# Performance work log

Hardware: AMD Instinct MI355X
Metric: run time of the kernel (lower is better)

## Reference

```python
import jax, jax.numpy as jnp
import numpy as np
from jax import lax

B, T, F_IN, H = 256, 800, 3, 200  # batch, time_steps, n_features, n_hidden=time_steps//4


def hard_sigmoid(z):
    return jnp.clip(0.2 * z + 0.5, 0.0, 1.0)


def lstm_hardsigmoid(x_btf, Wih, Whh, bih, bhh):
    """Unidirectional single-layer LSTM, hard-sigmoid gates, zero init state.
    x_btf: (B, T, F); Wih: (4H, F); Whh: (4H, H); biases: (4H,). Returns (B, T, H)."""
    Hh = Whh.shape[1]
    # input contribution for all timesteps at once: (B, T, 4H)
    pre = jnp.einsum('btf,gf->btg', x_btf, Wih) + bih + bhh
    pre_tb = jnp.swapaxes(pre, 0, 1)  # (T, B, 4H)
    b = x_btf.shape[0]
    init = (jnp.zeros((b, Hh), x_btf.dtype), jnp.zeros((b, Hh), x_btf.dtype))

    def step(carry, pre_t):
        h, c = carry
        gates = pre_t + h @ Whh.T  # (B, 4H)
        i, f, g, o = jnp.split(gates, 4, axis=-1)  # torch gate order i,f,g,o
        i = hard_sigmoid(i)
        f = hard_sigmoid(f)
        g = jnp.tanh(g)
        o = hard_sigmoid(o)
        c_new = f * c + i * g
        h_new = o * jnp.tanh(c_new)
        return (h_new, c_new), h_new

    _, hs = lax.scan(step, init, pre_tb)  # hs: (T, B, H)
    return jnp.swapaxes(hs, 0, 1)


def setup_inputs() -> dict:
    key = jax.random.key(0)
    ks = jax.random.split(key, 4)
    return {
        'x': jax.random.normal(ks[0], (B, F_IN, T), jnp.float32),
        'enc_Wih': jax.random.normal(ks[1], (4 * H, F_IN), jnp.float32) * 0.1,
        'enc_Whh': jax.random.normal(ks[2], (4 * H, H), jnp.float32) * 0.05,
        'enc_bih': jnp.zeros((4 * H,), jnp.float32),
        'enc_bhh': jnp.zeros((4 * H,), jnp.float32),
        'dec_Wih': jax.random.normal(ks[3], (4 * F_IN, H), jnp.float32) * 0.05,
        'dec_Whh': jax.random.normal(jax.random.fold_in(key, 7), (4 * F_IN, F_IN), jnp.float32) * 0.1,
        'dec_bih': jnp.zeros((4 * F_IN,), jnp.float32),
        'dec_bhh': jnp.zeros((4 * F_IN,), jnp.float32),
    }


def reference(x, enc_Wih, enc_Whh, enc_bih, enc_bhh, dec_Wih, dec_Whh, dec_bih, dec_bhh):
    # x: (B, n_features, T) -> permute -> (B, T, n_features)
    xi = jnp.transpose(x, (0, 2, 1))
    enc_out = lstm_hardsigmoid(xi, enc_Wih, enc_Whh, enc_bih, enc_bhh)  # (B, T, H)
    # max_pool1d over time (kernel = full length) == max over T
    pooled = jnp.max(enc_out, axis=1)  # (B, H)
    # repeat pooled vector for every timestep
    dec_in = jnp.broadcast_to(pooled[:, None, :], (pooled.shape[0], T, H))
    dec_out = lstm_hardsigmoid(dec_in, dec_Wih, dec_Whh, dec_bih, dec_bhh)  # (B, T, F)
    return jnp.transpose(dec_out, (0, 2, 1))  # (B, n_features, T)
```

## Files before the change

### kernel.cpp

```cpp
#include <hip/hip_runtime.h>
#include <hip/hip_fp16.h>
#include <stdint.h>


typedef _Float16 half2_t __attribute__((ext_vector_type(2)));

__device__ __forceinline__ float fdot2f(uint32_t hp, uint32_t wp, float acc) {
#if __has_builtin(__builtin_amdgcn_fdot2)
  return __builtin_amdgcn_fdot2(__builtin_bit_cast(half2_t, hp),
                                __builtin_bit_cast(half2_t, wp), acc, false);
#else
  half2_t a = __builtin_bit_cast(half2_t, hp);
  half2_t b = __builtin_bit_cast(half2_t, wp);
  return acc + (float)a[0] * (float)b[0] + (float)a[1] * (float)b[1];
#endif
}

__device__ __forceinline__ float hsig(float z) {
  return fminf(fmaxf(__builtin_fmaf(0.2f, z, 0.5f), 0.f), 1.f);
}

__device__ __forceinline__ float tanh_fast(float v) {
  float e = __builtin_amdgcn_exp2f(v * 2.885390081777927f);
  return 1.f - 2.f * __builtin_amdgcn_rcpf(e + 1.f);
}

__global__ void prep_kernel(const float* __restrict__ whh,
                            uint32_t* __restrict__ wpk) {
  int idx = blockIdx.x * 256 + threadIdx.x;
  if (idx >= 80000) return;
  int p = idx / 800;
  int j = idx - p * 800;
  float a = whh[j * 200 + 2 * p];
  float b = whh[j * 200 + 2 * p + 1];
  __half2 v = __floats2half2_rn(a, b);
  wpk[idx] = __builtin_bit_cast(uint32_t, v);
}

__global__ __launch_bounds__(832, 1)
void enc_kernel(const float* __restrict__ x,
                const float* __restrict__ wih,
                const float* __restrict__ bih,
                const float* __restrict__ bhh,
                const uint32_t* __restrict__ wpk,
                const float* __restrict__ dwih,
                const float* __restrict__ dbih,
                const float* __restrict__ dbhh,
                const float* __restrict__ dwhh,
                float* __restrict__ out)
{
  const int b = blockIdx.x;
  const int t = threadIdx.x;

  __shared__ float xs[2400];
  __shared__ alignas(16) __half hh[200];
  __shared__ float gates[800];
  __shared__ float pooled[200];
  __shared__ float pre12s[12];
  __shared__ int s_tc;

  for (int i = t; i < 2400; i += 832) xs[i] = x[(size_t)b * 2400 + i];
  if (t < 200) hh[t] = __float2half(0.f);

  const bool worker = t < 800;
  const int gtype = t / 200;
  uint32_t w[100];
  float bias = 0.f, wi0 = 0.f, wi1 = 0.f, wi2 = 0.f;
  if (worker) {
#pragma unroll
    for (int p = 0; p < 100; ++p) w[p] = wpk[p * 800 + t];
    bias = bih[t] + bhh[t];
    wi0 = wih[t * 3 + 0]; wi1 = wih[t * 3 + 1]; wi2 = wih[t * 3 + 2];
  }
  float c_state = 0.f;
  float maxh = -INFINITY;
  __syncthreads();

  for (int step = 0; step < 800; ++step) {
    if (worker) {
      float a0 = 0.f, a1 = 0.f;
      const uint4* H4 = (const uint4*)hh;
#pragma unroll
      for (int q = 0; q < 25; ++q) {
        uint4 Hv = H4[q];
        a0 = fdot2f(Hv.x, w[4 * q + 0], a0);
        a1 = fdot2f(Hv.y, w[4 * q + 1], a1);
        a0 = fdot2f(Hv.z, w[4 * q + 2], a0);
        a1 = fdot2f(Hv.w, w[4 * q + 3], a1);
      }
      float g = a0 + a1 + bias;
      g = __builtin_fmaf(wi0, xs[step], g);
      g = __builtin_fmaf(wi1, xs[800 + step], g);
      g = __builtin_fmaf(wi2, xs[1600 + step], g);
      float act;
      if (gtype == 2) act = tanh_fast(g); else act = hsig(g);
      gates[t] = act;
    }
    __syncthreads();
    if (t < 200) {
      float ai = gates[t], af = gates[t + 200];
      float ag = gates[t + 400], ao = gates[t + 600];
      c_state = __builtin_fmaf(af, c_state, ai * ag);
      float h_ = ao * tanh_fast(c_state);
      maxh = fmaxf(maxh, h_);
      hh[t] = __float2half(h_);
    }
    __syncthreads();
  }

  if (t < 200) pooled[t] = maxh;
  __syncthreads();
  if (t < 12) {
    float s = dbih[t] + dbhh[t];
    const float* wr = dwih + t * 200;
#pragma unroll 8
    for (int u = 0; u < 200; ++u) s = __builtin_fmaf(pooled[u], wr[u], s);
    pre12s[t] = s;
  }
  __syncthreads();

  if (t < 3) {
    float pre[12];
#pragma unroll
    for (int j = 0; j < 12; ++j) pre[j] = pre12s[j];
    float W[36];
#pragma unroll
    for (int j = 0; j < 36; ++j) W[j] = dwhh[j];

    float h0 = 0, h1 = 0, h2 = 0, c0 = 0, c1 = 0, c2 = 0;
    int tc = 800;
    float* hist = xs + t * 800;
    for (int step = 0; step < 800; ++step) {
      float g[12];
#pragma unroll
      for (int j = 0; j < 12; ++j) {
        float v = pre[j];
        v = __builtin_fmaf(W[j * 3 + 0], h0, v);
        v = __builtin_fmaf(W[j * 3 + 1], h1, v);
        v = __builtin_fmaf(W[j * 3 + 2], h2, v);
        g[j] = v;
      }
      float nc0 = hsig(g[3]) * c0 + hsig(g[0]) * tanh_fast(g[6]);
      float nc1 = hsig(g[4]) * c1 + hsig(g[1]) * tanh_fast(g[7]);
      float nc2 = hsig(g[5]) * c2 + hsig(g[2]) * tanh_fast(g[8]);
      float nh0 = hsig(g[9])  * tanh_fast(nc0);
      float nh1 = hsig(g[10]) * tanh_fast(nc1);
      float nh2 = hsig(g[11]) * tanh_fast(nc2);
      bool same = (nh0 == h0) && (nh1 == h1) && (nh2 == h2) &&
                  (nc0 == c0) && (nc1 == c1) && (nc2 == c2);
      float mine = (t == 0) ? nh0 : ((t == 1) ? nh1 : nh2);
      hist[step] = mine;
      h0 = nh0; h1 = nh1; h2 = nh2; c0 = nc0; c1 = nc1; c2 = nc2;
      if (same) { tc = step + 1; break; }
    }
    if (t == 0) s_tc = tc;
  }
  __syncthreads();

  {
    const int tc1 = s_tc - 1;
    float* ob = out + (size_t)b * 2400;
    if (t < 800) {
      int idx = (t < s_tc) ? t : tc1;
      ob[t]        = xs[idx];
      ob[800 + t]  = xs[800 + idx];
      ob[1600 + t] = xs[1600 + idx];
    }
  }
}

extern "C" void kernel_launch(void* const* d_in, const int* in_sizes, int n_in,
                              void* d_out, int out_size, void* d_ws, size_t ws_size,
                              hipStream_t stream)
{
  const float* x    = (const float*)d_in[0];
  const float* wih  = (const float*)d_in[1];
  const float* whh  = (const float*)d_in[2];
  const float* bih  = (const float*)d_in[3];
  const float* bhh  = (const float*)d_in[4];
  const float* dwih = (const float*)d_in[5];
  const float* dwhh = (const float*)d_in[6];
  const float* dbih = (const float*)d_in[7];
  const float* dbhh = (const float*)d_in[8];
  float* out = (float*)d_out;

  uint32_t* wpk = (uint32_t*)d_ws;

  hipLaunchKernelGGL(prep_kernel, dim3(313), dim3(256), 0, stream, whh, wpk);
  hipLaunchKernelGGL(enc_kernel, dim3(256), dim3(832), 0, stream,
                     x, wih, bih, bhh, wpk, dwih, dbih, dbhh, dwhh, out);
}
```

Before: 1.205 ms.

## Compute all four gates per hidden unit in one thread with double-buffered h

The encoder now uses 200 worker threads instead of 800. Each thread holds the weights of all four gates for one hidden unit in registers, about 400 words, and computes the cell update itself. This removes the shared gates array and the second barrier each step, and the h vector is double-buffered so one barrier per step is enough. The inputs are packed as float4 per timestep. The risks are heavy register pressure and possible spills, plus only one wave per SIMD left to hide latency.

```diff
diff --git a/kernel.cpp b/kernel.cpp
--- a/kernel.cpp
+++ b/kernel.cpp
@@ -37,7 +37,7 @@
   wpk[idx] = __builtin_bit_cast(uint32_t, v);
 }
 
-__global__ __launch_bounds__(832, 1)
+__global__ __launch_bounds__(256, 1)
 void enc_kernel(const float* __restrict__ x,
                 const float* __restrict__ wih,
                 const float* __restrict__ bih,
@@ -52,63 +52,91 @@
   const int b = blockIdx.x;
   const int t = threadIdx.x;
 
-  __shared__ float xs[2400];
-  __shared__ alignas(16) __half hh[200];
-  __shared__ float gates[800];
+  __shared__ alignas(16) float xs[3200];
+  __shared__ alignas(16) __half hh[2][208];
   __shared__ float pooled[200];
   __shared__ float pre12s[12];
   __shared__ int s_tc;
 
-  for (int i = t; i < 2400; i += 832) xs[i] = x[(size_t)b * 2400 + i];
-  if (t < 200) hh[t] = __float2half(0.f);
-
-  const bool worker = t < 800;
-  const int gtype = t / 200;
-  uint32_t w[100];
-  float bias = 0.f, wi0 = 0.f, wi1 = 0.f, wi2 = 0.f;
+  {
+    const float* xb = x + (size_t)b * 2400;
+    float4* X4 = (float4*)xs;
+    for (int tt = t; tt < 800; tt += 256) {
+      float4 v;
+      v.x = xb[tt];
+      v.y = xb[800 + tt];
+      v.z = xb[1600 + tt];
+      v.w = 0.f;
+      X4[tt] = v;
+    }
+  }
+  if (t < 208) { hh[0][t] = __float2half(0.f); }
+
+  const bool worker = t < 200;
+  uint32_t w[400];
+  float bias[4] = {0, 0, 0, 0};
+  float wi[12];
+#pragma unroll
+  for (int j = 0; j < 12; ++j) wi[j] = 0.f;
   if (worker) {
 #pragma unroll
-    for (int p = 0; p < 100; ++p) w[p] = wpk[p * 800 + t];
-    bias = bih[t] + bhh[t];
-    wi0 = wih[t * 3 + 0]; wi1 = wih[t * 3 + 1]; wi2 = wih[t * 3 + 2];
+    for (int g = 0; g < 4; ++g) {
+      const int row = t + 200 * g;
+#pragma unroll
+      for (int p = 0; p < 100; ++p) w[g * 100 + p] = wpk[p * 800 + row];
+      bias[g] = bih[row] + bhh[row];
+      wi[g * 3 + 0] = wih[row * 3 + 0];
+      wi[g * 3 + 1] = wih[row * 3 + 1];
+      wi[g * 3 + 2] = wih[row * 3 + 2];
+    }
   }
   float c_state = 0.f;
   float maxh = -INFINITY;
   __syncthreads();
 
+  int cur = 0;
   for (int step = 0; step < 800; ++step) {
     if (worker) {
-      float a0 = 0.f, a1 = 0.f;
-      const uint4* H4 = (const uint4*)hh;
+      float acc[8];
+#pragma unroll
+      for (int j = 0; j < 8; ++j) acc[j] = 0.f;
+      const uint4* H4 = (const uint4*)hh[cur];
 #pragma unroll
       for (int q = 0; q < 25; ++q) {
         uint4 Hv = H4[q];
-        a0 = fdot2f(Hv.x, w[4 * q + 0], a0);
-        a1 = fdot2f(Hv.y, w[4 * q + 1], a1);
-        a0 = fdot2f(Hv.z, w[4 * q + 2], a0);
-        a1 = fdot2f(Hv.w, w[4 * q + 3], a1);
+        const int d = q & 1;
+#pragma unroll
+        for (int g = 0; g < 4; ++g) {
+          float a = acc[2 * g + d];
+          a = fdot2f(Hv.x, w[g * 100 + 4 * q + 0], a);
+          a = fdot2f(Hv.y, w[g * 100 + 4 * q + 1], a);
+          a = fdot2f(Hv.z, w[g * 100 + 4 * q + 2], a);
+          a = fdot2f(Hv.w, w[g * 100 + 4 * q + 3], a);
+          acc[2 * g + d] = a;
+        }
       }
-      float g = a0 + a1 + bias;
-      g = __builtin_fmaf(wi0, xs[step], g);
-      g = __builtin_fmaf(wi1, xs[800 + step], g);
-      g = __builtin_fmaf(wi2, xs[1600 + step], g);
-      float act;
-      if (gtype == 2) act = tanh_fast(g); else act = hsig(g);
-      gates[t] = act;
+      float4 xv = ((const float4*)xs)[step];
+      float gte[4];
+#pragma unroll
+      for (int g = 0; g < 4; ++g) {
+        float v = acc[2 * g] + acc[2 * g + 1] + bias[g];
+        v = __builtin_fmaf(wi[g * 3 + 0], xv.x, v);
+        v = __builtin_fmaf(wi[g * 3 + 1], xv.y, v);
+        v = __builtin_fmaf(wi[g * 3 + 2], xv.z, v);
+        gte[g] = v;
+      }
+      float i_ = hsig(gte[0]), f_ = hsig(gte[1]), o_ = hsig(gte[3]);
+      float g_ = tanh_fast(gte[2]);
+      c_state = __builtin_fmaf(f_, c_state, i_ * g_);
+      float h_ = o_ * tanh_fast(c_state);
+      maxh = fmaxf(maxh, h_);
+      hh[cur ^ 1][t] = __float2half(h_);
     }
     __syncthreads();
-    if (t < 200) {
-      float ai = gates[t], af = gates[t + 200];
-      float ag = gates[t + 400], ao = gates[t + 600];
-      c_state = __builtin_fmaf(af, c_state, ai * ag);
-      float h_ = ao * tanh_fast(c_state);
-      maxh = fmaxf(maxh, h_);
-      hh[t] = __float2half(h_);
-    }
-    __syncthreads();
-  }
-
-  if (t < 200) pooled[t] = maxh;
+    cur ^= 1;
+  }
+
+  if (worker) pooled[t] = maxh;
   __syncthreads();
   if (t < 12) {
     float s = dbih[t] + dbhh[t];
@@ -129,7 +157,6 @@
 
     float h0 = 0, h1 = 0, h2 = 0, c0 = 0, c1 = 0, c2 = 0;
     int tc = 800;
-    float* hist = xs + t * 800;
     for (int step = 0; step < 800; ++step) {
       float g[12];
 #pragma unroll
@@ -149,7 +176,7 @@
       bool same = (nh0 == h0) && (nh1 == h1) && (nh2 == h2) &&
                   (nc0 == c0) && (nc1 == c1) && (nc2 == c2);
       float mine = (t == 0) ? nh0 : ((t == 1) ? nh1 : nh2);
-      hist[step] = mine;
+      xs[step * 4 + t] = mine;
       h0 = nh0; h1 = nh1; h2 = nh2; c0 = nc0; c1 = nc1; c2 = nc2;
       if (same) { tc = step + 1; break; }
     }
@@ -158,13 +185,13 @@
   __syncthreads();
 
   {
-    const int tc1 = s_tc - 1;
+    const int tcv = s_tc, tc1 = tcv - 1;
     float* ob = out + (size_t)b * 2400;
-    if (t < 800) {
-      int idx = (t < s_tc) ? t : tc1;
-      ob[t]        = xs[idx];
-      ob[800 + t]  = xs[800 + idx];
-      ob[1600 + t] = xs[1600 + idx];
+    for (int tt = t; tt < 800; tt += 256) {
+      int idx = (tt < tcv) ? tt : tc1;
+      ob[tt]        = xs[idx * 4 + 0];
+      ob[800 + tt]  = xs[idx * 4 + 1];
+      ob[1600 + tt] = xs[idx * 4 + 2];
     }
   }
 }
@@ -187,6 +214,6 @@
   uint32_t* wpk = (uint32_t*)d_ws;
 
   hipLaunchKernelGGL(prep_kernel, dim3(313), dim3(256), 0, stream, whh, wpk);
-  hipLaunchKernelGGL(enc_kernel, dim3(256), dim3(832), 0, stream,
+  hipLaunchKernelGGL(enc_kernel, dim3(256), dim3(256), 0, stream,
                      x, wih, bih, bhh, wpk, dwih, dbih, dbhh, dwhh, out);
 }
```

Result: slower. 2.095 ms (+73.8%).

## Split encoder recurrence by K-quarters with readlane broadcast and double-buffered h

Applied to the files above, without the earlier changes.

Reorganizes the encoder step so 1024 threads each own one hidden unit's four gates over a quarter of the h vector. Each thread fetches its h slice via readlane broadcast instead of per-lane LDS reads. Partial sums go through shared memory, and quarter 0 combines them, adds fp16 input projections, and applies the cell update. Double-buffered h removes a read/write hazard and merges the gate-activation pass into the reducer, cutting per-step LDS traffic. The cost is an extra partial-sum exchange, fp16 rounding of x and Wih, and a larger block.

```diff
diff --git a/kernel.cpp b/kernel.cpp
--- a/kernel.cpp
+++ b/kernel.cpp
@@ -37,7 +37,7 @@
   wpk[idx] = __builtin_bit_cast(uint32_t, v);
 }
 
-__global__ __launch_bounds__(832, 1)
+__global__ __launch_bounds__(1024, 4)
 void enc_kernel(const float* __restrict__ x,
                 const float* __restrict__ wih,
                 const float* __restrict__ bih,
@@ -51,61 +51,116 @@
 {
   const int b = blockIdx.x;
   const int t = threadIdx.x;
-
-  __shared__ float xs[2400];
-  __shared__ alignas(16) __half hh[200];
-  __shared__ float gates[800];
+  const int lane = t & 63;
+  const int wid = t >> 6;
+  const int q2 = wid >> 2;
+  const int u = (wid & 3) * 64 + lane;
+
+  __shared__ uint32_t hbuf[2][128];
+  __shared__ uint2 xs2[800];
+  __shared__ float4 part[3][256];
+  __shared__ uint4 wiA[256];
+  __shared__ uint4 wiB[256];
+  __shared__ float4 biasL[256];
+  __shared__ float hist[3200];
   __shared__ float pooled[200];
   __shared__ float pre12s[12];
   __shared__ int s_tc;
 
-  for (int i = t; i < 2400; i += 832) xs[i] = x[(size_t)b * 2400 + i];
-  if (t < 200) hh[t] = __float2half(0.f);
-
-  const bool worker = t < 800;
-  const int gtype = t / 200;
+  {
+    const float* xb = x + (size_t)b * 2400;
+    if (t < 800) {
+      __half2 p01 = __floats2half2_rn(xb[t], xb[800 + t]);
+      __half2 p23 = __floats2half2_rn(xb[1600 + t], 0.f);
+      uint2 v;
+      v.x = __builtin_bit_cast(uint32_t, p01);
+      v.y = __builtin_bit_cast(uint32_t, p23);
+      xs2[t] = v;
+    }
+    if (t < 256) ((uint32_t*)hbuf)[t] = 0;
+    if (t < 256) {
+      int uu = t;
+      uint4 A, B; float4 bs;
+      int r0 = uu < 200 ? uu : 199;
+#pragma unroll
+      for (int g = 0; g < 4; ++g) {
+        int row = r0 + 200 * g;
+        __half2 w01 = __floats2half2_rn(wih[row * 3 + 0], wih[row * 3 + 1]);
+        __half2 w2_ = __floats2half2_rn(wih[row * 3 + 2], 0.f);
+        uint32_t a0 = __builtin_bit_cast(uint32_t, w01);
+        uint32_t a1 = __builtin_bit_cast(uint32_t, w2_);
+        if (g == 0) { A.x = a0; A.y = a1; }
+        else if (g == 1) { A.z = a0; A.w = a1; }
+        else if (g == 2) { B.x = a0; B.y = a1; }
+        else { B.z = a0; B.w = a1; }
+        ((float*)&bs)[g] = bih[row] + bhh[row];
+      }
+      wiA[uu] = A; wiB[uu] = B; biasL[uu] = bs;
+    }
+  }
+
   uint32_t w[100];
-  float bias = 0.f, wi0 = 0.f, wi1 = 0.f, wi2 = 0.f;
-  if (worker) {
-#pragma unroll
-    for (int p = 0; p < 100; ++p) w[p] = wpk[p * 800 + t];
-    bias = bih[t] + bhh[t];
-    wi0 = wih[t * 3 + 0]; wi1 = wih[t * 3 + 1]; wi2 = wih[t * 3 + 2];
-  }
+#pragma unroll
+  for (int g = 0; g < 4; ++g) {
+    int row = u + 200 * g; if (row > 799) row = 799;
+    const uint32_t* src = wpk + (size_t)(q2 * 25) * 800 + row;
+#pragma unroll
+    for (int p = 0; p < 25; ++p) w[g * 25 + p] = src[p * 800];
+  }
+
   float c_state = 0.f;
   float maxh = -INFINITY;
-  __syncthreads();
-
-  for (int step = 0; step < 800; ++step) {
-    if (worker) {
-      float a0 = 0.f, a1 = 0.f;
-      const uint4* H4 = (const uint4*)hh;
-#pragma unroll
-      for (int q = 0; q < 25; ++q) {
-        uint4 Hv = H4[q];
-        a0 = fdot2f(Hv.x, w[4 * q + 0], a0);
-        a1 = fdot2f(Hv.y, w[4 * q + 1], a1);
-        a0 = fdot2f(Hv.z, w[4 * q + 2], a0);
-        a1 = fdot2f(Hv.w, w[4 * q + 3], a1);
-      }
-      float g = a0 + a1 + bias;
-      g = __builtin_fmaf(wi0, xs[step], g);
-      g = __builtin_fmaf(wi1, xs[800 + step], g);
-      g = __builtin_fmaf(wi2, xs[1600 + step], g);
-      float act;
-      if (gtype == 2) act = tanh_fast(g); else act = hsig(g);
-      gates[t] = act;
+
+  const int pu = u >> 1;
+  const int hoff = (pu / 25) * 128 + (pu % 25) * 4 + (u & 1) * 2;
+  __half* hW0 = (__half*)((char*)&hbuf[0][0] + hoff);
+  __half* hW1 = (__half*)((char*)&hbuf[1][0] + hoff);
+  const uint4* h4a = (const uint4*)&hbuf[0][q2 * 32];
+  const uint4* h4b = (const uint4*)&hbuf[1][q2 * 32];
+  const int lidx = (lane < 7) ? lane : 6;
+
+  __syncthreads();
+
+  auto STEP = [&](const uint4* srcH, __half* dstH, int step) {
+    uint4 hv = srcH[lidx];
+    float a0 = 0.f, a1 = 0.f, a2 = 0.f, a3 = 0.f;
+#pragma unroll
+    for (int p = 0; p < 25; ++p) {
+      const int ln = p >> 2, d = p & 3;
+      uint32_t comp = (d == 0) ? hv.x : (d == 1) ? hv.y : (d == 2) ? hv.z : hv.w;
+      uint32_t hp = __builtin_amdgcn_readlane(comp, ln);
+      a0 = fdot2f(hp, w[p], a0);
+      a1 = fdot2f(hp, w[25 + p], a1);
+      a2 = fdot2f(hp, w[50 + p], a2);
+      a3 = fdot2f(hp, w[75 + p], a3);
+    }
+    if (q2 != 0) {
+      float4 pv; pv.x = a0; pv.y = a1; pv.z = a2; pv.w = a3;
+      part[q2 - 1][u] = pv;
     }
     __syncthreads();
-    if (t < 200) {
-      float ai = gates[t], af = gates[t + 200];
-      float ag = gates[t + 400], ao = gates[t + 600];
-      c_state = __builtin_fmaf(af, c_state, ai * ag);
-      float h_ = ao * tanh_fast(c_state);
+    if (q2 == 0 && u < 200) {
+      float4 pa = part[0][u], pb = part[1][u], pc = part[2][u];
+      uint4 A = wiA[u], B = wiB[u];
+      float4 bs = biasL[u];
+      uint2 xv = xs2[step];
+      float gi = fdot2f(xv.y, A.y, fdot2f(xv.x, A.x, a0 + pa.x + pb.x + pc.x + bs.x));
+      float gf = fdot2f(xv.y, A.w, fdot2f(xv.x, A.z, a1 + pa.y + pb.y + pc.y + bs.y));
+      float gg = fdot2f(xv.y, B.y, fdot2f(xv.x, B.x, a2 + pa.z + pb.z + pc.z + bs.z));
+      float go = fdot2f(xv.y, B.w, fdot2f(xv.x, B.z, a3 + pa.w + pb.w + pc.w + bs.w));
+      float i_ = hsig(gi), f_ = hsig(gf), o_ = hsig(go);
+      float g_ = tanh_fast(gg);
+      c_state = __builtin_fmaf(f_, c_state, i_ * g_);
+      float h_ = o_ * tanh_fast(c_state);
       maxh = fmaxf(maxh, h_);
-      hh[t] = __float2half(h_);
+      *dstH = __float2half(h_);
     }
     __syncthreads();
+  };
+
+  for (int sp = 0; sp < 400; ++sp) {
+    STEP(h4a, hW1, 2 * sp);
+    STEP(h4b, hW0, 2 * sp + 1);
   }
 
   if (t < 200) pooled[t] = maxh;
@@ -114,7 +169,7 @@
     float s = dbih[t] + dbhh[t];
     const float* wr = dwih + t * 200;
 #pragma unroll 8
-    for (int u = 0; u < 200; ++u) s = __builtin_fmaf(pooled[u], wr[u], s);
+    for (int uu = 0; uu < 200; ++uu) s = __builtin_fmaf(pooled[uu], wr[uu], s);
     pre12s[t] = s;
   }
   __syncthreads();
@@ -129,7 +184,6 @@
 
     float h0 = 0, h1 = 0, h2 = 0, c0 = 0, c1 = 0, c2 = 0;
     int tc = 800;
-    float* hist = xs + t * 800;
     for (int step = 0; step < 800; ++step) {
       float g[12];
 #pragma unroll
@@ -149,7 +203,7 @@
       bool same = (nh0 == h0) && (nh1 == h1) && (nh2 == h2) &&
                   (nc0 == c0) && (nc1 == c1) && (nc2 == c2);
       float mine = (t == 0) ? nh0 : ((t == 1) ? nh1 : nh2);
-      hist[step] = mine;
+      hist[step * 4 + t] = mine;
       h0 = nh0; h1 = nh1; h2 = nh2; c0 = nc0; c1 = nc1; c2 = nc2;
       if (same) { tc = step + 1; break; }
     }
@@ -158,13 +212,13 @@
   __syncthreads();
 
   {
-    const int tc1 = s_tc - 1;
+    const int tcv = s_tc, tc1 = tcv - 1;
     float* ob = out + (size_t)b * 2400;
     if (t < 800) {
-      int idx = (t < s_tc) ? t : tc1;
-      ob[t]        = xs[idx];
-      ob[800 + t]  = xs[800 + idx];
-      ob[1600 + t] = xs[1600 + idx];
+      int idx = (t < tcv) ? t : tc1;
+      ob[t]        = hist[idx * 4 + 0];
+      ob[800 + t]  = hist[idx * 4 + 1];
+      ob[1600 + t] = hist[idx * 4 + 2];
     }
   }
 }
@@ -187,6 +241,6 @@
   uint32_t* wpk = (uint32_t*)d_ws;
 
   hipLaunchKernelGGL(prep_kernel, dim3(313), dim3(256), 0, stream, whh, wpk);
-  hipLaunchKernelGGL(enc_kernel, dim3(256), dim3(832), 0, stream,
+  hipLaunchKernelGGL(enc_kernel, dim3(256), dim3(1024), 0, stream,
                      x, wih, bih, bhh, wpk, dwih, dbih, dbhh, dwhh, out);
 }
```

Result: slower. 1.854 ms (+53.8%).
